# Kernel optimization log

Measured on AMD Instinct MI355X. Metric: run time of the kernel, lower is better.

Reference implementation:

```python
import jax, jax.numpy as jnp
import numpy as np

# Static problem sizes (must match setup_inputs).
B = 4096      # number of events (unique batch_idx values)
NPER = 2000   # hits per event; NPER == maxhits -> deterministic arange selection
D = 4         # clustering-space dimensionality
EPS = 1e-6


def setup_inputs() -> dict:
    key = jax.random.key(0)
    clust_space = jax.random.normal(key, (B * NPER, D), dtype=jnp.float32)
    # Sorted, equal-sized groups: batch_idx = [0]*NPER, [1]*NPER, ...
    batch_idx = jnp.repeat(jnp.arange(B, dtype=jnp.int32), NPER)
    return {"clust_space": clust_space, "batch_idx": batch_idx}


def reference(clust_space, batch_idx):
    # batch_idx is sorted with equal group sizes, so the per-event Python loop
    # of the original module is a reshape to [B, NPER, D].
    coords = clust_space.reshape(B, NPER, D)
    # Per-event mean and centered coordinates.
    c = coords - coords.mean(axis=1, keepdims=True)            # [B, NPER, D]
    # Covariance: mean over hits of outer products -> [B, D, D] (symmetric).
    cov = jnp.einsum('bnd,bne->bde', c, c) / NPER
    # Symmetric real matrix: eigvalsh == real part of torch.linalg.eig output.
    eig = jnp.linalg.eigvalsh(cov)                             # [B, D]
    pen = jnp.log((eig.mean(axis=-1) / (eig.min(axis=-1) + EPS) - 1.0) ** 2 + 1.0)
    # Original sums the per-event penalties into a scalar loss.
    return pen.sum()
```

## Files before the change

kernel.cpp:

```cpp
#include <hip/hip_runtime.h>
#include <hip/hip_bf16.h>
#include <math.h>

#define NB    4096
#define NPER  2000
#define NDIM  4
#define EPS   1e-6
#define BLOCK 256

__device__ double jacobi_pen(double a00, double a01, double a02, double a03,
                             double a11, double a12, double a13,
                             double a22, double a23, double a33) {
    double A[4][4] = {
        {a00, a01, a02, a03},
        {a01, a11, a12, a13},
        {a02, a12, a22, a23},
        {a03, a13, a23, a33}
    };
    for (int sweep = 0; sweep < 15; ++sweep) {
        double off = A[0][1]*A[0][1] + A[0][2]*A[0][2] + A[0][3]*A[0][3]
                   + A[1][2]*A[1][2] + A[1][3]*A[1][3] + A[2][3]*A[2][3];
        if (off < 1e-26) break;
        for (int p = 0; p < 3; ++p) {
            for (int q = p + 1; q < 4; ++q) {
                double apq = A[p][q];
                if (fabs(apq) < 1e-300) continue;
                double app = A[p][p], aqq = A[q][q];
                double tau = (aqq - app) / (2.0 * apq);
                double t = (tau >= 0.0 ? 1.0 : -1.0) /
                           (fabs(tau) + sqrt(1.0 + tau * tau));
                double c = 1.0 / sqrt(1.0 + t * t);
                double s = t * c;
                for (int k = 0; k < 4; ++k) {
                    double akp = A[k][p], akq = A[k][q];
                    A[k][p] = c * akp - s * akq;
                    A[k][q] = s * akp + c * akq;
                }
                for (int k = 0; k < 4; ++k) {
                    double apk = A[p][k], aqk = A[q][k];
                    A[p][k] = c * apk - s * aqk;
                    A[q][k] = s * apk + c * aqk;
                }
                A[p][q] = 0.0;
                A[q][p] = 0.0;
            }
        }
    }
    double e0 = A[0][0], e1 = A[1][1], e2 = A[2][2], e3 = A[3][3];
    double mean = 0.25 * (e0 + e1 + e2 + e3);
    double mn = fmin(fmin(e0, e1), fmin(e2, e3));
    double r = mean / (mn + EPS) - 1.0;
    return log(r * r + 1.0);
}

__global__ __launch_bounds__(BLOCK)
void event_pen_kernel(const float4* __restrict__ cs, float* __restrict__ pen_out) {
    const int b = blockIdx.x;
    const float4* __restrict__ p = cs + (size_t)b * NPER;

    float s0 = 0.f, s1 = 0.f, s2 = 0.f, s3 = 0.f;
    float m00 = 0.f, m01 = 0.f, m02 = 0.f, m03 = 0.f;
    float m11 = 0.f, m12 = 0.f, m13 = 0.f;
    float m22 = 0.f, m23 = 0.f, m33 = 0.f;

    for (int i = threadIdx.x; i < NPER; i += BLOCK) {
        float4 v = p[i];
        s0 += v.x; s1 += v.y; s2 += v.z; s3 += v.w;
        m00 += v.x * v.x; m01 += v.x * v.y; m02 += v.x * v.z; m03 += v.x * v.w;
        m11 += v.y * v.y; m12 += v.y * v.z; m13 += v.y * v.w;
        m22 += v.z * v.z; m23 += v.z * v.w;
        m33 += v.w * v.w;
    }

    float vals[14] = {s0, s1, s2, s3,
                      m00, m01, m02, m03, m11, m12, m13, m22, m23, m33};

    __shared__ float red[BLOCK / 64][14];
    const int lane = threadIdx.x & 63;
    const int wave = threadIdx.x >> 6;

#pragma unroll
    for (int i = 0; i < 14; ++i) {
        float v = vals[i];
#pragma unroll
        for (int off = 32; off > 0; off >>= 1)
            v += __shfl_down(v, off, 64);
        if (lane == 0) red[wave][i] = v;
    }
    __syncthreads();

    if (threadIdx.x == 0) {
        double t[14];
#pragma unroll
        for (int i = 0; i < 14; ++i) {
            float acc = red[0][i];
            for (int w = 1; w < BLOCK / 64; ++w) acc += red[w][i];
            t[i] = (double)acc;
        }
        const double invN = 1.0 / (double)NPER;
        double mu0 = t[0] * invN, mu1 = t[1] * invN,
               mu2 = t[2] * invN, mu3 = t[3] * invN;
        double c00 = t[4]  * invN - mu0 * mu0;
        double c01 = t[5]  * invN - mu0 * mu1;
        double c02 = t[6]  * invN - mu0 * mu2;
        double c03 = t[7]  * invN - mu0 * mu3;
        double c11 = t[8]  * invN - mu1 * mu1;
        double c12 = t[9]  * invN - mu1 * mu2;
        double c13 = t[10] * invN - mu1 * mu3;
        double c22 = t[11] * invN - mu2 * mu2;
        double c23 = t[12] * invN - mu2 * mu3;
        double c33 = t[13] * invN - mu3 * mu3;

        pen_out[b] = (float)jacobi_pen(c00, c01, c02, c03,
                                       c11, c12, c13, c22, c23, c33);
    }
}

__global__ __launch_bounds__(BLOCK)
void reduce_pen_kernel(const float* __restrict__ pen, float* __restrict__ out) {
    double s = 0.0;
    for (int i = threadIdx.x; i < NB; i += BLOCK)
        s += (double)pen[i];

    __shared__ double red[BLOCK / 64];
    const int lane = threadIdx.x & 63;
    const int wave = threadIdx.x >> 6;

#pragma unroll
    for (int off = 32; off > 0; off >>= 1)
        s += __shfl_down(s, off, 64);
    if (lane == 0) red[wave] = s;
    __syncthreads();

    if (threadIdx.x == 0) {
        double tot = red[0];
        for (int w = 1; w < BLOCK / 64; ++w) tot += red[w];
        out[0] = (float)tot;
    }
}

extern "C" void kernel_launch(void* const* d_in, const int* in_sizes, int n_in,
                              void* d_out, int out_size, void* d_ws, size_t ws_size,
                              hipStream_t stream) {
    const float4* cs = (const float4*)d_in[0];
    float* pen = (float*)d_ws;
    float* out = (float*)d_out;

    event_pen_kernel<<<NB, BLOCK, 0, stream>>>(cs, pen);
    reduce_pen_kernel<<<1, BLOCK, 0, stream>>>(pen, out);
}
```

Before: 236.0 us.

## Assign one wave per event and move eigen-solve into a per-thread batched kernel

The moments pass now maps each event to a single 64-lane wave, removing the shared-memory cross-wave reduction and block barrier, and writes the 14 raw moments to workspace. A second kernel runs the Jacobi eigen-solve with one thread per event, replacing the single thread per block that previously serialized it, and accumulates penalties with a wave reduction plus atomicAdd. This takes the serial FP64 Jacobi tail off the bandwidth-bound streaming pass. In exchange it adds a memset and a workspace round trip, cuts the sweep cap to 10, and makes the final float atomic sum order nondeterministic.

```diff
diff --git a/kernel.cpp b/kernel.cpp
--- a/kernel.cpp
+++ b/kernel.cpp
@@ -4,58 +4,13 @@
 
 #define NB    4096
 #define NPER  2000
-#define NDIM  4
 #define EPS   1e-6
-#define BLOCK 256
 
-__device__ double jacobi_pen(double a00, double a01, double a02, double a03,
-                             double a11, double a12, double a13,
-                             double a22, double a23, double a33) {
-    double A[4][4] = {
-        {a00, a01, a02, a03},
-        {a01, a11, a12, a13},
-        {a02, a12, a22, a23},
-        {a03, a13, a23, a33}
-    };
-    for (int sweep = 0; sweep < 15; ++sweep) {
-        double off = A[0][1]*A[0][1] + A[0][2]*A[0][2] + A[0][3]*A[0][3]
-                   + A[1][2]*A[1][2] + A[1][3]*A[1][3] + A[2][3]*A[2][3];
-        if (off < 1e-26) break;
-        for (int p = 0; p < 3; ++p) {
-            for (int q = p + 1; q < 4; ++q) {
-                double apq = A[p][q];
-                if (fabs(apq) < 1e-300) continue;
-                double app = A[p][p], aqq = A[q][q];
-                double tau = (aqq - app) / (2.0 * apq);
-                double t = (tau >= 0.0 ? 1.0 : -1.0) /
-                           (fabs(tau) + sqrt(1.0 + tau * tau));
-                double c = 1.0 / sqrt(1.0 + t * t);
-                double s = t * c;
-                for (int k = 0; k < 4; ++k) {
-                    double akp = A[k][p], akq = A[k][q];
-                    A[k][p] = c * akp - s * akq;
-                    A[k][q] = s * akp + c * akq;
-                }
-                for (int k = 0; k < 4; ++k) {
-                    double apk = A[p][k], aqk = A[q][k];
-                    A[p][k] = c * apk - s * aqk;
-                    A[q][k] = s * apk + c * aqk;
-                }
-                A[p][q] = 0.0;
-                A[q][p] = 0.0;
-            }
-        }
-    }
-    double e0 = A[0][0], e1 = A[1][1], e2 = A[2][2], e3 = A[3][3];
-    double mean = 0.25 * (e0 + e1 + e2 + e3);
-    double mn = fmin(fmin(e0, e1), fmin(e2, e3));
-    double r = mean / (mn + EPS) - 1.0;
-    return log(r * r + 1.0);
-}
-
-__global__ __launch_bounds__(BLOCK)
-void event_pen_kernel(const float4* __restrict__ cs, float* __restrict__ pen_out) {
-    const int b = blockIdx.x;
+__global__ __launch_bounds__(256)
+void moments_kernel(const float4* __restrict__ cs, float* __restrict__ mom) {
+    const int wave = threadIdx.x >> 6;
+    const int lane = threadIdx.x & 63;
+    const int b = blockIdx.x * 4 + wave;
     const float4* __restrict__ p = cs + (size_t)b * NPER;
 
     float s0 = 0.f, s1 = 0.f, s2 = 0.f, s3 = 0.f;
@@ -63,8 +18,17 @@
     float m11 = 0.f, m12 = 0.f, m13 = 0.f;
     float m22 = 0.f, m23 = 0.f, m33 = 0.f;
 
-    for (int i = threadIdx.x; i < NPER; i += BLOCK) {
-        float4 v = p[i];
+#pragma unroll 4
+    for (int i = 0; i < 31; ++i) {
+        float4 v = p[i * 64 + lane];
+        s0 += v.x; s1 += v.y; s2 += v.z; s3 += v.w;
+        m00 += v.x * v.x; m01 += v.x * v.y; m02 += v.x * v.z; m03 += v.x * v.w;
+        m11 += v.y * v.y; m12 += v.y * v.z; m13 += v.y * v.w;
+        m22 += v.z * v.z; m23 += v.z * v.w;
+        m33 += v.w * v.w;
+    }
+    if (lane < 16) {
+        float4 v = p[1984 + lane];
         s0 += v.x; s1 += v.y; s2 += v.z; s3 += v.w;
         m00 += v.x * v.x; m01 += v.x * v.y; m02 += v.x * v.z; m03 += v.x * v.w;
         m11 += v.y * v.y; m12 += v.y * v.z; m13 += v.y * v.w;
@@ -74,68 +38,98 @@
 
     float vals[14] = {s0, s1, s2, s3,
                       m00, m01, m02, m03, m11, m12, m13, m22, m23, m33};
-
-    __shared__ float red[BLOCK / 64][14];
-    const int lane = threadIdx.x & 63;
-    const int wave = threadIdx.x >> 6;
-
 #pragma unroll
-    for (int i = 0; i < 14; ++i) {
-        float v = vals[i];
+    for (int j = 0; j < 14; ++j) {
+        float v = vals[j];
 #pragma unroll
         for (int off = 32; off > 0; off >>= 1)
             v += __shfl_down(v, off, 64);
-        if (lane == 0) red[wave][i] = v;
+        vals[j] = v;
     }
-    __syncthreads();
 
-    if (threadIdx.x == 0) {
-        double t[14];
+    if (lane == 0) {
+        float* o = mom + (size_t)b * 16;
 #pragma unroll
-        for (int i = 0; i < 14; ++i) {
-            float acc = red[0][i];
-            for (int w = 1; w < BLOCK / 64; ++w) acc += red[w][i];
-            t[i] = (double)acc;
-        }
-        const double invN = 1.0 / (double)NPER;
-        double mu0 = t[0] * invN, mu1 = t[1] * invN,
-               mu2 = t[2] * invN, mu3 = t[3] * invN;
-        double c00 = t[4]  * invN - mu0 * mu0;
-        double c01 = t[5]  * invN - mu0 * mu1;
-        double c02 = t[6]  * invN - mu0 * mu2;
-        double c03 = t[7]  * invN - mu0 * mu3;
-        double c11 = t[8]  * invN - mu1 * mu1;
-        double c12 = t[9]  * invN - mu1 * mu2;
-        double c13 = t[10] * invN - mu1 * mu3;
-        double c22 = t[11] * invN - mu2 * mu2;
-        double c23 = t[12] * invN - mu2 * mu3;
-        double c33 = t[13] * invN - mu3 * mu3;
-
-        pen_out[b] = (float)jacobi_pen(c00, c01, c02, c03,
-                                       c11, c12, c13, c22, c23, c33);
+        for (int j = 0; j < 14; ++j) o[j] = vals[j];
     }
 }
 
-__global__ __launch_bounds__(BLOCK)
-void reduce_pen_kernel(const float* __restrict__ pen, float* __restrict__ out) {
-    double s = 0.0;
-    for (int i = threadIdx.x; i < NB; i += BLOCK)
-        s += (double)pen[i];
+__global__ __launch_bounds__(256)
+void pen_kernel(const float* __restrict__ mom, float* __restrict__ out) {
+    const int b = blockIdx.x * 256 + threadIdx.x;
+    const float* m = mom + (size_t)b * 16;
 
-    __shared__ double red[BLOCK / 64];
+    double t[14];
+#pragma unroll
+    for (int j = 0; j < 14; ++j) t[j] = (double)m[j];
+
+    const double invN = 1.0 / (double)NPER;
+    double mu0 = t[0] * invN, mu1 = t[1] * invN,
+           mu2 = t[2] * invN, mu3 = t[3] * invN;
+
+    double A[4][4];
+    A[0][0] = t[4]  * invN - mu0 * mu0;
+    A[0][1] = A[1][0] = t[5]  * invN - mu0 * mu1;
+    A[0][2] = A[2][0] = t[6]  * invN - mu0 * mu2;
+    A[0][3] = A[3][0] = t[7]  * invN - mu0 * mu3;
+    A[1][1] = t[8]  * invN - mu1 * mu1;
+    A[1][2] = A[2][1] = t[9]  * invN - mu1 * mu2;
+    A[1][3] = A[3][1] = t[10] * invN - mu1 * mu3;
+    A[2][2] = t[11] * invN - mu2 * mu2;
+    A[2][3] = A[3][2] = t[12] * invN - mu2 * mu3;
+    A[3][3] = t[13] * invN - mu3 * mu3;
+
+    for (int sweep = 0; sweep < 10; ++sweep) {
+        double off = A[0][1]*A[0][1] + A[0][2]*A[0][2] + A[0][3]*A[0][3]
+                   + A[1][2]*A[1][2] + A[1][3]*A[1][3] + A[2][3]*A[2][3];
+        if (__all(off < 1e-26)) break;
+#pragma unroll
+        for (int p = 0; p < 3; ++p) {
+#pragma unroll
+            for (int q = p + 1; q < 4; ++q) {
+                double apq = A[p][q];
+                if (fabs(apq) > 1e-300) {
+                    double tau = (A[q][q] - A[p][p]) / (2.0 * apq);
+                    double tt = (tau >= 0.0 ? 1.0 : -1.0) /
+                                (fabs(tau) + sqrt(1.0 + tau * tau));
+                    double c = 1.0 / sqrt(1.0 + tt * tt);
+                    double s = tt * c;
+#pragma unroll
+                    for (int k = 0; k < 4; ++k) {
+                        double akp = A[k][p], akq = A[k][q];
+                        A[k][p] = c * akp - s * akq;
+                        A[k][q] = s * akp + c * akq;
+                    }
+#pragma unroll
+                    for (int k = 0; k < 4; ++k) {
+                        double apk = A[p][k], aqk = A[q][k];
+                        A[p][k] = c * apk - s * aqk;
+                        A[q][k] = s * apk + c * aqk;
+                    }
+                    A[p][q] = 0.0;
+                    A[q][p] = 0.0;
+                }
+            }
+        }
+    }
+
+    double e0 = A[0][0], e1 = A[1][1], e2 = A[2][2], e3 = A[3][3];
+    double mean = 0.25 * (e0 + e1 + e2 + e3);
+    double mn = fmin(fmin(e0, e1), fmin(e2, e3));
+    double r = mean / (mn + EPS) - 1.0;
+    float pen = (float)log(r * r + 1.0);
+
     const int lane = threadIdx.x & 63;
-    const int wave = threadIdx.x >> 6;
-
+    const int wv = threadIdx.x >> 6;
+    __shared__ float red[4];
 #pragma unroll
     for (int off = 32; off > 0; off >>= 1)
-        s += __shfl_down(s, off, 64);
-    if (lane == 0) red[wave] = s;
+        pen += __shfl_down(pen, off, 64);
+    if (lane == 0) red[wv] = pen;
     __syncthreads();
-
     if (threadIdx.x == 0) {
-        double tot = red[0];
-        for (int w = 1; w < BLOCK / 64; ++w) tot += red[w];
-        out[0] = (float)tot;
+        float s = red[0] + red[1] + red[2] + red[3];
+        atomicAdd(out, s);
     }
 }
 
@@ -143,9 +137,10 @@
                               void* d_out, int out_size, void* d_ws, size_t ws_size,
                               hipStream_t stream) {
     const float4* cs = (const float4*)d_in[0];
-    float* pen = (float*)d_ws;
+    float* mom = (float*)d_ws;
     float* out = (float*)d_out;
 
-    event_pen_kernel<<<NB, BLOCK, 0, stream>>>(cs, pen);
-    reduce_pen_kernel<<<1, BLOCK, 0, stream>>>(pen, out);
+    hipMemsetAsync(out, 0, sizeof(float), stream);
+    moments_kernel<<<NB / 4, 256, 0, stream>>>(cs, mom);
+    pen_kernel<<<NB / 256, 256, 0, stream>>>(mom, out);
 }
```

Result: faster. 216.9 us (-8.1%).
